# Kernel optimization log

Measured on AMD Instinct MI355X. Metric: run time of the kernel, lower is better.

The kernel has to match this reference:

```python
import jax, jax.numpy as jnp
import numpy as np

SPANS = [15, 9, 5]   # processed largest-first, matching sorted(span_groups, reverse=True)
DEPTH = 2
TOL = 1.5


def _rmsnorm(x, eps=1e-5):
    return x * jax.lax.rsqrt(jnp.mean(x * x, axis=-1, keepdims=True) + eps)


def _block(m, g, Wi, Wz, Wdt, bdt, alog, Wo, Wyg):
    """Dual-input gated selective-scan block (stand-in for create_multihead_block
    block_type='dual_input'): match stream runs a diagonal SSM scan over window
    tokens, gated by the geometry stream; both streams are residually updated."""
    u = _rmsnorm(m) @ Wi                              # [P,L,C]
    z = jax.nn.silu(_rmsnorm(g) @ Wz)                 # [P,L,C] geom gate
    delta = jax.nn.softplus(u @ Wdt + bdt)            # [P,L,C]
    decay = jnp.exp(delta * (-jnp.exp(alog)))         # [P,L,C]
    x_in = delta * u

    def step(h, inp):
        d, xi = inp
        h = d * h + xi
        return h, h

    _, hs = jax.lax.scan(step, jnp.zeros_like(x_in[:, 0]),
                         (jnp.swapaxes(decay, 0, 1), jnp.swapaxes(x_in, 0, 1)))
    y = jnp.swapaxes(hs, 0, 1) * z                    # [P,L,C]
    return m + y @ Wo, g + jax.nn.silu(y @ Wyg)


def _sample(feat_flat, ys, xs, H, W):
    """Bilinear sampling, align_corners=True, padding_mode='zeros'.
    feat_flat: [C, H*W]; ys, xs: [L] float coords. Returns [L, C]."""
    y0 = jnp.floor(ys); x0 = jnp.floor(xs)
    wy = ys - y0; wx = xs - x0

    def tap(yi, xi):
        valid = ((yi >= 0) & (yi <= H - 1) & (xi >= 0) & (xi <= W - 1)).astype(feat_flat.dtype)
        idx = (jnp.clip(yi, 0, H - 1).astype(jnp.int32) * W
               + jnp.clip(xi, 0, W - 1).astype(jnp.int32))
        return feat_flat[:, idx] * valid              # [C,L]

    v = (tap(y0, x0) * (1 - wy) * (1 - wx) + tap(y0, x0 + 1) * (1 - wy) * wx
         + tap(y0 + 1, x0) * wy * (1 - wx) + tap(y0 + 1, x0 + 1) * wy * wx)
    return v.T


def _process_side(feat_m, feat_g, flow, sx, sy, params):
    B, C, H, W = feat_m.shape
    G = feat_g.shape[1]
    Wi, Wz, Wdt, bdt, alog, Wo, Wyg = params
    dt = feat_m.dtype
    bb, yy, xx = [a.ravel() for a in jnp.meshgrid(jnp.arange(B), jnp.arange(H), jnp.arange(W), indexing='ij')]
    # flow-shifted sub-pixel window centers, clamped (flow[...,0]=dx, flow[...,1]=dy)
    cy = jnp.clip(yy.astype(dt) + flow[bb, yy, xx, 1], 0, H - 1)
    cx = jnp.clip(xx.astype(dt) + flow[bb, yy, xx, 0], 0, W - 1)
    avg = ((sx + sy) * 0.5).ravel()
    assigned = jnp.zeros(avg.shape, dtype=bool)
    fm = feat_m.reshape(B, C, H * W)
    fg = feat_g.reshape(B, G, H * W)
    out_m = jnp.zeros((B * H * W, C), dt)
    out_g = jnp.zeros((B * H * W, G), dt)
    wsum = jnp.zeros((B * H * W,), dt)
    for si, s in enumerate(SPANS):
        # span-group mask; positions claimed by a larger span are excluded
        mask = (jnp.abs(avg - s) < TOL) & (~assigned)
        assigned = assigned | mask
        h = s // 2
        dy, dx = [a.ravel() for a in jnp.meshgrid(jnp.arange(-h, h + 1), jnp.arange(-h, h + 1), indexing='ij')]
        dist = jnp.sqrt((dy * dy + dx * dx).astype(dt))
        pw = jnp.exp(-dist / (s / 2.0))
        pw = pw / pw.sum()                             # normalized distance weights [L]
        ys = cy[:, None] + dy[None, :].astype(dt)      # [P,L]
        xs = cx[:, None] + dx[None, :].astype(dt)
        wm = jax.vmap(lambda b, y, x: _sample(fm[b], y, x, H, W))(bb, ys, xs)  # [P,L,C]
        wg = jax.vmap(lambda b, y, x: _sample(fg[b], y, x, H, W))(bb, ys, xs)  # [P,L,G]
        for d in range(DEPTH):
            wm, wg = _block(wm, wg, Wi[si, d], Wz[si, d], Wdt[si, d], bdt[si, d], alog[si, d], Wo[si, d], Wyg[si, d])
        # scatter-accumulate around the integer center position
        ty = yy[:, None] + dy[None, :]
        tx = xx[:, None] + dx[None, :]
        valid = ((ty >= 0) & (ty < H) & (tx >= 0) & (tx < W)).astype(dt)
        w = pw[None, :] * mask[:, None].astype(dt) * valid           # [P,L]
        idx = bb[:, None] * (H * W) + jnp.clip(ty, 0, H - 1) * W + jnp.clip(tx, 0, W - 1)
        out_m = out_m.at[idx.ravel()].add((wm * w[..., None]).reshape(-1, C))
        out_g = out_g.at[idx.ravel()].add((wg * w[..., None]).reshape(-1, G))
        wsum = wsum.at[idx.ravel()].add(w.ravel())
    ws = jnp.maximum(wsum, 1e-6)[:, None]
    om = (out_m / ws).reshape(B, H, W, C).transpose(0, 3, 1, 2)
    og = (out_g / ws).reshape(B, H, W, G).transpose(0, 3, 1, 2)
    return om, og


def setup_inputs() -> dict:
    key = jax.random.key(0)
    ks = jax.random.split(key, 18)
    B, C, G, H, W = 1, 128, 64, 28, 28
    f32 = jnp.float32
    d = {}
    d['feat_match_0'] = jax.random.normal(ks[0], (B, C, H, W), f32)
    d['feat_match_1'] = jax.random.normal(ks[1], (B, C, H, W), f32)
    d['feat_geom_0'] = jax.random.normal(ks[2], (B, G, H, W), f32)
    d['feat_geom_1'] = jax.random.normal(ks[3], (B, G, H, W), f32)
    d['flow_map_0'] = 1.5 * jax.random.normal(ks[4], (B, H, W, 4), f32)
    d['flow_map_1'] = 1.5 * jax.random.normal(ks[5], (B, H, W, 4), f32)
    # spans in [3, 17) so each span group {5, 9, 15} is populated
    d['adaptive_spans_x_0'] = 3.0 + 14.0 * jax.random.uniform(ks[6], (B, H, W), f32)
    d['adaptive_spans_y_0'] = 3.0 + 14.0 * jax.random.uniform(ks[7], (B, H, W), f32)
    d['adaptive_spans_x_1'] = 3.0 + 14.0 * jax.random.uniform(ks[8], (B, H, W), f32)
    d['adaptive_spans_y_1'] = 3.0 + 14.0 * jax.random.uniform(ks[9], (B, H, W), f32)
    # per-span (order [15,9,5]) x per-depth block parameters
    d['W_in'] = jax.random.normal(ks[10], (3, DEPTH, C, C), f32) / np.sqrt(C).astype(np.float32)
    d['W_z'] = jax.random.normal(ks[11], (3, DEPTH, G, C), f32) / np.sqrt(G).astype(np.float32)
    d['W_dt'] = jax.random.normal(ks[12], (3, DEPTH, C, C), f32) / np.sqrt(C).astype(np.float32)
    d['b_dt'] = 0.1 * jax.random.normal(ks[13], (3, DEPTH, C), f32)
    d['a_log'] = 0.1 * jax.random.normal(ks[14], (3, DEPTH, C), f32)
    d['W_out'] = jax.random.normal(ks[15], (3, DEPTH, C, C), f32) / np.sqrt(C).astype(np.float32)
    d['W_yg'] = jax.random.normal(ks[16], (3, DEPTH, C, G), f32) / np.sqrt(C).astype(np.float32)
    return d


def reference(feat_match_0, feat_match_1, feat_geom_0, feat_geom_1,
              flow_map_0, flow_map_1,
              adaptive_spans_x_0, adaptive_spans_y_0,
              adaptive_spans_x_1, adaptive_spans_y_1,
              W_in, W_z, W_dt, b_dt, a_log, W_out, W_yg):
    params = (W_in, W_z, W_dt, b_dt, a_log, W_out, W_yg)
    m0, g0 = _process_side(feat_match_0, feat_geom_0, flow_map_0[..., :2],
                           adaptive_spans_x_0, adaptive_spans_y_0, params)
    m1, g1 = _process_side(feat_match_1, feat_geom_1, flow_map_1[..., :2],
                           adaptive_spans_x_1, adaptive_spans_y_1, params)
    return m0, m1, g0, g1
```

## Files before the change

kernel.cpp:

```cpp
#include <hip/hip_runtime.h>
#include <math.h>

typedef short s16x8 __attribute__((ext_vector_type(8)));
typedef unsigned short u16x8v __attribute__((ext_vector_type(8)));
typedef float f32x4 __attribute__((ext_vector_type(4)));
typedef _Float16 h2 __attribute__((ext_vector_type(2)));

#define HH 28
#define WW 28
#define PP 784
#define CC 128
#define GG 64
#define MT 48
#define NH 3
#define AST 136
#define GSTB 72

#define OFF_FMT0 0
#define OFF_FMT1 100352
#define OFF_FGT0 200704
#define OFF_FGT1 250880
#define OFF_ACCM0 301056
#define OFF_ACCM1 401408
#define OFF_ACCG0 501760
#define OFF_ACCG1 551936
#define OFF_ACCW0 602112
#define OFF_ACCW1 602896
#define ACC_FLOATS 302624
#define OFF_CNT   603680
#define OFF_CNT2  603704
#define OFF_JOB   603728
#define OFF_WB    605296

#define WIB 0
#define WZB 98304
#define WDB 147456
#define WOB 245760
#define WYB 344064

struct KArgs {
  const float* fm[2]; const float* fg[2];
  const float* flow[2]; const float* sx[2]; const float* sy[2];
  const float* Wi; const float* Wz; const float* Wdt; const float* bdt;
  const float* alog; const float* Wo; const float* Wyg;
  float* fmT[2]; float* fgT[2];
  float* accm[2]; float* accg[2]; float* accw[2];
  int* cnt; int* cnt2; int* job;
  unsigned short* wb;
  float* out;
};

__device__ __forceinline__ int span_group(float avg, int& s) {
  if (fabsf(avg - 15.f) < 1.5f) { s = 15; return 0; }
  if (fabsf(avg - 9.f)  < 1.5f) { s = 9;  return 1; }
  if (fabsf(avg - 5.f)  < 1.5f) { s = 5;  return 2; }
  s = 0; return 3;
}

__device__ __forceinline__ float fast_silu(float x) {
  return x * __builtin_amdgcn_rcpf(1.f + __expf(-x));
}

__device__ __forceinline__ unsigned short f2bf(float f) {
  unsigned u = __float_as_uint(f);
  unsigned r = (u + 0x7fffu + ((u >> 16) & 1u)) >> 16;
  return (unsigned short)r;
}
__device__ __forceinline__ float b2f(unsigned short u) {
  return __uint_as_float(((unsigned)u) << 16);
}

__device__ __forceinline__ void atomic_pk2(_Float16* base, float x, float y) {
  h2 v; v[0] = (_Float16)x; v[1] = (_Float16)y;
#if __has_builtin(__builtin_amdgcn_global_atomic_fadd_v2f16)
  __builtin_amdgcn_global_atomic_fadd_v2f16((h2*)base, v);
#else
  unsigned* a = (unsigned*)base;
  unsigned old = *a, assumed;
  do {
    assumed = old;
    h2 cur = *(h2*)&assumed;
    h2 nw; nw[0] = cur[0] + v[0]; nw[1] = cur[1] + v[1];
    old = atomicCAS(a, assumed, *(unsigned*)&nw);
  } while (old != assumed);
#endif
}

#define MFMA(A_, B_, C_) __builtin_amdgcn_mfma_f32_16x16x32_bf16((A_), (B_), (C_), 0, 0, 0)

__global__ void k_zero(float* p, int n) {
  int j = blockIdx.x * 256 + threadIdx.x;
  if (j < n) p[j] = 0.f;
}

__global__ void k_prep(KArgs a) {
  int j = blockIdx.x * 256 + threadIdx.x;
  int side = j / 150528; int r = j - side * 150528;
  int p = r / 192; int ch = r - p * 192;
  if (ch < CC) a.fmT[side][p * CC + ch] = a.fm[side][ch * PP + p];
  else         a.fgT[side][p * GG + (ch - CC)] = a.fg[side][(ch - CC) * PP + p];
}

__global__ void k_prepw(KArgs a) {
  int j = blockIdx.x * 256 + threadIdx.x;
  unsigned short* wb = a.wb;
  if (j < 98304) {
    int set = j >> 14, r = j & 16383; int o = r >> 7, c = r & 127;
    wb[WIB + j] = f2bf(a.Wi[set * 16384 + c * 128 + o]);
  } else if (j < 147456) {
    int r = j - 98304; int set = r >> 13, rr = r & 8191; int o = rr >> 6, c = rr & 63;
    wb[WZB + r] = f2bf(a.Wz[set * 8192 + c * 128 + o]);
  } else if (j < 245760) {
  } else if (j < 344064) {
    int r = j - 245760; int set = r >> 14, rr = r & 16383; int o = rr >> 7, c = rr & 127;
    wb[WOB + r] = f2bf(a.Wo[set * 16384 + c * 128 + o]);
  } else {
    int r = j - 344064; int set = r >> 13, rr = r & 8191; int o = rr >> 7, c = rr & 127;
    wb[WYB + r] = f2bf(a.Wyg[set * 8192 + c * 64 + o]);
  }
}

__global__ void k_prepwid(KArgs a) {
  __shared__ float wi_row[128];
  const int set = blockIdx.x, i = blockIdx.y, o = threadIdx.x;
  wi_row[o] = a.Wi[set * 16384 + i * 128 + o];
  __syncthreads();
  float acc = 0.f;
#pragma unroll 4
  for (int m = 0; m < 128; ++m) acc = fmaf(wi_row[m], a.Wdt[set * 16384 + m * 128 + o], acc);
  a.wb[WDB + set * 16384 + o * 128 + i] = f2bf(acc);
}

__global__ void k_count(KArgs a) {
  int j = blockIdx.x * 256 + threadIdx.x;
  if (j >= 2 * PP) return;
  a.job[j] = -1;
  int side = j / PP, p = j - side * PP;
  float avg = 0.5f * (a.sx[side][p] + a.sy[side][p]);
  int s; int g = span_group(avg, s);
  if (g < 3) {
    int py = p / WW, px = p - py * WW;
    int region = (py / 14) * 4 + px / 7;
    atomicAdd(&a.cnt[region * 3 + g], 1);
  }
}

__global__ void k_assign(KArgs a) {
  int j = blockIdx.x * 256 + threadIdx.x;
  if (j >= 2 * PP) return;
  int side = j / PP, p = j - side * PP;
  float avg = 0.5f * (a.sx[side][p] + a.sy[side][p]);
  int s; int g = span_group(avg, s);
  if (g < 3) {
    int py = p / WW, px = p - py * WW;
    int region = (py / 14) * 4 + px / 7;
    int base = 0;
    for (int gg = 0; gg < g; ++gg) base += a.cnt[region * 3 + gg];
    int rank = base + atomicAdd(&a.cnt2[region * 3 + g], 1);
    a.job[region + 8 * rank] = (side << 10) | p;
  }
}

__global__ void k_fin(KArgs a) {
  int j = blockIdx.x * 256 + threadIdx.x;
  int side = j / 150528; int r = j - side * 150528;
  int p = r / 192; int ch = r - p * 192;
  float inv = 1.f / fmaxf(a.accw[side][p], 1e-6f);
  if (ch < CC) {
    const _Float16* amh = (const _Float16*)a.accm[side];
    a.out[side * 100352 + ch * PP + p] = (float)amh[p * CC + ch] * inv;
  } else {
    const _Float16* agh = (const _Float16*)a.accg[side];
    a.out[200704 + side * 50176 + (ch - CC) * PP + p] = (float)agh[p * GG + (ch - CC)] * inv;
  }
}

__launch_bounds__(256, 3)
__global__ void k_main(KArgs a) {
  __shared__ __align__(16) unsigned short mres[MT * AST];
  __shared__ __align__(16) unsigned short gres[MT * GSTB];
  __shared__ __align__(16) unsigned short bufA[MT * AST];
  __shared__ __align__(16) unsigned short bufB[MT * GSTB];
  __shared__ float hs[2 * CC];
  __shared__ float na_s[2 * CC];
  __shared__ float bb_s[2 * CC];
  __shared__ float pw_l[228];
  __shared__ int   tap_i[MT * 4];
  __shared__ float tap_w[MT * 4];
  __shared__ int   sc_i[MT];
  __shared__ float sc_w[MT];
  __shared__ float red[4];

  const int tid = threadIdx.x;
  const int job = a.job[blockIdx.x];
  if (job < 0) return;
  const int side = job >> 10, p = job & 1023;
  const float avg = 0.5f * (a.sx[side][p] + a.sy[side][p]);
  int s; const int si = span_group(avg, s);
  const int hspan = s >> 1, L = s * s;
  const int py = p / WW, px = p - py * WW;
  const float fdx = a.flow[side][p * 4 + 0], fdy = a.flow[side][p * 4 + 1];
  const float cy = fminf(fmaxf((float)py + fdy, 0.f), (float)(HH - 1));
  const float cx = fminf(fmaxf((float)px + fdx, 0.f), (float)(WW - 1));
  const float* fmT = a.fmT[side]; const float* fgT = a.fgT[side];
  _Float16* accm_h = (_Float16*)a.accm[side];
  _Float16* accg_h = (_Float16*)a.accg[side];
  float* accw = a.accw[side];

  const unsigned short* wb = a.wb;
  const int wv = tid >> 6, l = tid & 63, lm = l & 15, g = l >> 4;
  const int o0 = 32 * wv + lm, o1 = o0 + 16, og = 16 * wv + lm;
  const int ttk = tid >> 3, c8 = tid & 7;

  { const int d2 = tid >> 7, c2 = tid & 127;
    na_s[tid] = -__expf(a.alog[(si * 2 + d2) * CC + c2]);
    bb_s[tid] = a.bdt[(si * 2 + d2) * CC + c2];
    hs[tid] = 0.f; }
  if (tid < L) {
    const int dyi = tid / s - hspan, dxi = tid % s - hspan;
    pw_l[tid] = __expf(-sqrtf((float)(dyi * dyi + dxi * dxi)) / (0.5f * (float)s));
  }
  __syncthreads();
  { float v = (tid < L) ? pw_l[tid] : 0.f;
#pragma unroll
    for (int off = 32; off > 0; off >>= 1) v += __shfl_xor(v, off);
    if ((tid & 63) == 0) red[tid >> 6] = v; }
  __syncthreads();
  { const float pinv = 1.f / (red[0] + red[1] + red[2] + red[3]);
    if (tid < L) pw_l[tid] *= pinv; }
  __syncthreads();

  const int nt = (L + MT - 1) / MT;

  for (int t = 0; t < nt; ++t) {
    const int t0 = t * MT;
    const int tlen = min(MT, L - t0);
    if (tid < MT) {
      const int t2 = t0 + tid;
      if (t2 < L) {
        const int tq = t2 / s;
        const int dyi = tq - hspan, dxi = (t2 - tq * s) - hspan;
        const float ys = cy + (float)dyi, xs = cx + (float)dxi;
        const float y0f = floorf(ys), x0f = floorf(xs);
        const float wy = ys - y0f, wx = xs - x0f;
        const int y0 = (int)y0f, x0 = (int)x0f;
#pragma unroll
        for (int k = 0; k < 4; ++k) {
          const int yi = y0 + (k >> 1), xi = x0 + (k & 1);
          const bool v = (yi >= 0) && (yi < HH) && (xi >= 0) && (xi < WW);
          const int yc = min(max(yi, 0), HH - 1), xc = min(max(xi, 0), WW - 1);
          tap_i[tid * 4 + k] = yc * WW + xc;
          const float wgt = ((k >> 1) ? wy : 1.f - wy) * ((k & 1) ? wx : 1.f - wx);
          tap_w[tid * 4 + k] = v ? wgt : 0.f;
        }
        const int ty = py + dyi, tx = px + dxi;
        const bool sv = (ty >= 0) && (ty < HH) && (tx >= 0) && (tx < WW);
        const int sid2 = sv ? ty * WW + tx : 0;
        const float sw = sv ? pw_l[t2] : 0.f;
        sc_i[tid] = sid2; sc_w[tid] = sw;
        if (sw != 0.f) atomicAdd(&accw[sid2], sw);
      } else {
#pragma unroll
        for (int k = 0; k < 4; ++k) { tap_i[tid * 4 + k] = 0; tap_w[tid * 4 + k] = 0.f; }
        sc_i[tid] = 0; sc_w[tid] = 0.f;
      }
    }
    __syncthreads();
    for (int tk = ttk; tk < MT; tk += 32) {
      const int* ti = &tap_i[tk * 4]; const float* tw = &tap_w[tk * 4];
      f32x4 am0 = {0.f,0.f,0.f,0.f}, am1 = am0, am2 = am0, am3 = am0;
      f32x4 ag0 = am0, ag1 = am0;
#pragma unroll
      for (int k2 = 0; k2 < 4; ++k2) {
        const float w = tw[k2];
        const float* pm = &fmT[ti[k2] * CC + c8 * 16];
        am0 += w * *(const f32x4*)&pm[0];
        am1 += w * *(const f32x4*)&pm[4];
        am2 += w * *(const f32x4*)&pm[8];
        am3 += w * *(const f32x4*)&pm[12];
        const float* pg = &fgT[ti[k2] * GG + c8 * 8];
        ag0 += w * *(const f32x4*)&pg[0];
        ag1 += w * *(const f32x4*)&pg[4];
      }
      u16x8v w0, w1, wg;
#pragma unroll
      for (int j = 0; j < 4; ++j) {
        w0[j] = f2bf(am0[j]); w0[4 + j] = f2bf(am1[j]);
        w1[j] = f2bf(am2[j]); w1[4 + j] = f2bf(am3[j]);
        wg[j] = f2bf(ag0[j]); wg[4 + j] = f2bf(ag1[j]);
      }
      *(u16x8v*)&mres[tk * AST + c8 * 16] = w0;
      *(u16x8v*)&mres[tk * AST + c8 * 16 + 8] = w1;
      *(u16x8v*)&gres[tk * GSTB + c8 * 8] = wg;
    }

    for (int d = 0; d < 2; ++d) {
      const unsigned short* Wib  = wb + WIB + (si * 2 + d) * 16384;
      const unsigned short* Widb = wb + WDB + (si * 2 + d) * 16384;
      const unsigned short* Wzb  = wb + WZB + (si * 2 + d) * 8192;
      const unsigned short* Wob  = wb + WOB + (si * 2 + d) * 16384;
      const unsigned short* Wyb  = wb + WYB + (si * 2 + d) * 8192;
      if (d == 1) __syncthreads();
      for (int tk = ttk; tk < MT; tk += 32) {
        u16x8v m0 = *(const u16x8v*)&mres[tk * AST + c8 * 16];
        u16x8v m1 = *(const u16x8v*)&mres[tk * AST + c8 * 16 + 8];
        u16x8v gv = *(const u16x8v*)&gres[tk * GSTB + c8 * 8];
        float mv[16], gvf[8];
#pragma unroll
        for (int k = 0; k < 8; ++k) { mv[k] = b2f(m0[k]); mv[8 + k] = b2f(m1[k]); gvf[k] = b2f(gv[k]); }
        float ssm = 0.f, ssg = 0.f;
#pragma unroll
        for (int k = 0; k < 16; ++k) ssm = fmaf(mv[k], mv[k], ssm);
#pragma unroll
        for (int k = 0; k < 8; ++k) ssg = fmaf(gvf[k], gvf[k], ssg);
#pragma unroll
        for (int off = 4; off > 0; off >>= 1) { ssm += __shfl_xor(ssm, off); ssg += __shfl_xor(ssg, off); }
        const float sm = rsqrtf(ssm * (1.f / CC) + 1e-5f);
        const float sgs = rsqrtf(ssg * (1.f / GG) + 1e-5f);
        u16x8v xa, xb, gx;
#pragma unroll
        for (int k = 0; k < 8; ++k) { xa[k] = f2bf(mv[k] * sm); xb[k] = f2bf(mv[8 + k] * sm); gx[k] = f2bf(gvf[k] * sgs); }
        *(u16x8v*)&bufA[tk * AST + c8 * 16] = xa;
        *(u16x8v*)&bufA[tk * AST + c8 * 16 + 8] = xb;
        *(u16x8v*)&bufB[tk * GSTB + c8 * 8] = gx;
      }
      __syncthreads();
      f32x4 u[NH][2], dt[NH][2], z[NH][2];
#pragma unroll
      for (int h = 0; h < NH; ++h)
#pragma unroll
        for (int j2 = 0; j2 < 2; ++j2) { u[h][j2] = (f32x4){0.f,0.f,0.f,0.f}; dt[h][j2] = (f32x4){0.f,0.f,0.f,0.f}; z[h][j2] = (f32x4){0.f,0.f,0.f,0.f}; }
#pragma unroll
      for (int ss = 0; ss < 4; ++ss) {
        const int c0 = 32 * ss + g * 8;
        const s16x8 bW0 = *(const s16x8*)&Wib[o0 * 128 + c0];
        const s16x8 bW1 = *(const s16x8*)&Wib[o1 * 128 + c0];
        const s16x8 bD0 = *(const s16x8*)&Widb[o0 * 128 + c0];
        const s16x8 bD1 = *(const s16x8*)&Widb[o1 * 128 + c0];
#pragma unroll
        for (int h = 0; h < NH; ++h) {
          s16x8 av = *(const s16x8*)&bufA[(h * 16 + lm) * AST + c0];
          u[h][0]  = MFMA(av, bW0, u[h][0]);
          u[h][1]  = MFMA(av, bW1, u[h][1]);
          dt[h][0] = MFMA(av, bD0, dt[h][0]);
          dt[h][1] = MFMA(av, bD1, dt[h][1]);
        }
      }
#pragma unroll
      for (int ss = 0; ss < 2; ++ss) {
        const int c0 = 32 * ss + g * 8;
        const s16x8 bZ0 = *(const s16x8*)&Wzb[o0 * 64 + c0];
        const s16x8 bZ1 = *(const s16x8*)&Wzb[o1 * 64 + c0];
#pragma unroll
        for (int h = 0; h < NH; ++h) {
          s16x8 gv2 = *(const s16x8*)&bufB[(h * 16 + lm) * GSTB + c0];
          z[h][0] = MFMA(gv2, bZ0, z[h][0]);
          z[h][1] = MFMA(gv2, bZ1, z[h][1]);
        }
      }
#pragma unroll
      for (int h = 0; h < NH; ++h)
#pragma unroll
        for (int j2 = 0; j2 < 2; ++j2)
#pragma unroll
          for (int r = 0; r < 4; ++r) z[h][j2][r] = fast_silu(z[h][j2][r]);

#pragma unroll
      for (int j2 = 0; j2 < 2; ++j2) {
        const int oc = j2 ? o1 : o0;
        const float bb = bb_s[d * CC + oc], na = na_s[d * CC + oc];
        float hcar = hs[d * CC + oc];
#pragma unroll
        for (int h = 0; h < NH; ++h) {
          float Pl[4], Dl[4]; float P = 0.f, D = 1.f;
#pragma unroll
          for (int r = 0; r < 4; ++r) {
            const float x = dt[h][j2][r] + bb;
            float dlt = fmaxf(x, 0.f) + __logf(1.f + __expf(-fabsf(x)));
            float dec = __expf(dlt * na), xin = dlt * u[h][j2][r];
            if (h * 16 + 4 * g + r >= tlen) { dec = 1.f; xin = 0.f; }
            P = dec * P + xin; D *= dec; Pl[r] = P; Dl[r] = D;
          }
          float Pi = P, Di = D;
          { float pa = __shfl_up(Pi, 16), da = __shfl_up(Di, 16);
            if (g >= 1) { Pi = Di * pa + Pi; Di *= da; }
            pa = __shfl_up(Pi, 32); da = __shfl_up(Di, 32);
            if (g >= 2) { Pi = Di * pa + Pi; Di *= da; } }
          float Pe = __shfl_up(Pi, 16), De = __shfl_up(Di, 16);
          if (g == 0) { Pe = 0.f; De = 1.f; }
          const float cr = De * hcar + Pe;
          const float Pf = __shfl(Pi, 48 + lm), Df = __shfl(Di, 48 + lm);
#pragma unroll
          for (int r = 0; r < 4; ++r) z[h][j2][r] = (Dl[r] * cr + Pl[r]) * z[h][j2][r];
          hcar = Df * hcar + Pf;
        }
        if (g == 0) hs[d * CC + oc] = hcar;
      }
      __syncthreads();
#pragma unroll
      for (int h = 0; h < NH; ++h)
#pragma unroll
        for (int r = 0; r < 4; ++r) {
          const int rw = h * 16 + 4 * g + r;
          bufA[rw * AST + o0] = f2bf(z[h][0][r]);
          bufA[rw * AST + o1] = f2bf(z[h][1][r]);
        }
      __syncthreads();
      f32x4 dm[NH][2], dgv[NH];
#pragma unroll
      for (int h = 0; h < NH; ++h) { dm[h][0] = (f32x4){0.f,0.f,0.f,0.f}; dm[h][1] = (f32x4){0.f,0.f,0.f,0.f}; dgv[h] = (f32x4){0.f,0.f,0.f,0.f}; }
#pragma unroll
      for (int ss = 0; ss < 4; ++ss) {
        const int c0 = 32 * ss + g * 8;
        const s16x8 bO0 = *(const s16x8*)&Wob[o0 * 128 + c0];
        const s16x8 bO1 = *(const s16x8*)&Wob[o1 * 128 + c0];
        const s16x8 bY  = *(const s16x8*)&Wyb[og * 128 + c0];
#pragma unroll
        for (int h = 0; h < NH; ++h) {
          s16x8 av = *(const s16x8*)&bufA[(h * 16 + lm) * AST + c0];
          dm[h][0] = MFMA(av, bO0, dm[h][0]);
          dm[h][1] = MFMA(av, bO1, dm[h][1]);
          dgv[h]   = MFMA(av, bY, dgv[h]);
        }
      }
      if (d == 0) {
#pragma unroll
        for (int h = 0; h < NH; ++h)
#pragma unroll
          for (int r = 0; r < 4; ++r) {
            const int rw = h * 16 + 4 * g + r;
            mres[rw * AST + o0] = f2bf(b2f(mres[rw * AST + o0]) + dm[h][0][r]);
            mres[rw * AST + o1] = f2bf(b2f(mres[rw * AST + o1]) + dm[h][1][r]);
            gres[rw * GSTB + og] = f2bf(b2f(gres[rw * GSTB + og]) + fast_silu(dgv[h][r]));
          }
      } else {
        const bool evn = (lm & 1) == 0;
#pragma unroll
        for (int h = 0; h < NH; ++h)
#pragma unroll
          for (int r = 0; r < 4; ++r) {
            const int rw = h * 16 + 4 * g + r;
            const float w = sc_w[rw];
            const int tgt = sc_i[rw];
            const float vm0 = (b2f(mres[rw * AST + o0]) + dm[h][0][r]) * w;
            const float vm1 = (b2f(mres[rw * AST + o1]) + dm[h][1][r]) * w;
            const float vg  = (b2f(gres[rw * GSTB + og]) + fast_silu(dgv[h][r])) * w;
            const float pm0 = __shfl_xor(vm0, 1);
            const float pm1 = __shfl_xor(vm1, 1);
            const float pg  = __shfl_xor(vg, 1);
            if (w != 0.f) {
              if (evn) {
                atomic_pk2(accm_h + tgt * CC + o0, vm0, pm0);
                atomic_pk2(accg_h + tgt * GG + og, vg, pg);
              } else {
                atomic_pk2(accm_h + tgt * CC + o1 - 1, pm1, vm1);
              }
            }
          }
      }
    }
    __syncthreads();
  }
}

extern "C" void kernel_launch(void* const* d_in, const int* in_sizes, int n_in,
                              void* d_out, int out_size, void* d_ws, size_t ws_size,
                              hipStream_t stream) {
  (void)in_sizes; (void)n_in; (void)out_size; (void)ws_size;
  float* ws = (float*)d_ws;
  KArgs a;
  a.fm[0]  = (const float*)d_in[0]; a.fm[1]  = (const float*)d_in[1];
  a.fg[0]  = (const float*)d_in[2]; a.fg[1]  = (const float*)d_in[3];
  a.flow[0] = (const float*)d_in[4]; a.flow[1] = (const float*)d_in[5];
  a.sx[0] = (const float*)d_in[6]; a.sy[0] = (const float*)d_in[7];
  a.sx[1] = (const float*)d_in[8]; a.sy[1] = (const float*)d_in[9];
  a.Wi  = (const float*)d_in[10]; a.Wz   = (const float*)d_in[11];
  a.Wdt = (const float*)d_in[12]; a.bdt  = (const float*)d_in[13];
  a.alog = (const float*)d_in[14]; a.Wo  = (const float*)d_in[15];
  a.Wyg = (const float*)d_in[16];
  a.fmT[0] = ws + OFF_FMT0; a.fmT[1] = ws + OFF_FMT1;
  a.fgT[0] = ws + OFF_FGT0; a.fgT[1] = ws + OFF_FGT1;
  a.accm[0] = ws + OFF_ACCM0; a.accm[1] = ws + OFF_ACCM1;
  a.accg[0] = ws + OFF_ACCG0; a.accg[1] = ws + OFF_ACCG1;
  a.accw[0] = ws + OFF_ACCW0; a.accw[1] = ws + OFF_ACCW1;
  a.cnt  = (int*)(ws + OFF_CNT);
  a.cnt2 = (int*)(ws + OFF_CNT2);
  a.job  = (int*)(ws + OFF_JOB);
  a.wb   = (unsigned short*)(ws + OFF_WB);
  a.out = (float*)d_out;

  k_zero<<<1183, 256, 0, stream>>>(ws + OFF_ACCM0, ACC_FLOATS);
  k_zero<<<1, 256, 0, stream>>>(ws + OFF_CNT, 48);
  k_prep<<<1176, 256, 0, stream>>>(a);
  k_prepw<<<1536, 256, 0, stream>>>(a);
  k_prepwid<<<dim3(6, 128), 128, 0, stream>>>(a);
  k_count<<<7, 256, 0, stream>>>(a);
  k_assign<<<7, 256, 0, stream>>>(a);
  k_main<<<1568, 256, 0, stream>>>(a);
  k_fin<<<1176, 256, 0, stream>>>(a);
}
```

Baseline: 201.2 us.

## Double k_main block to 512 threads with one output column tile per wave

Raises k_main from 256 to 512 threads so each of 8 waves owns a single 16-column output slice instead of two, halving per-thread MFMA accumulators and weight loads. The W_yg GEMM and geometry updates run only on the first four waves, and the gather and norm loops become single iterations per thread. The aim is more waves in flight and lower register pressure per thread for latency hiding. The cost is idle waves during the geometry-stream work and more threads contending at barriers.

```diff
diff --git a/kernel.cpp b/kernel.cpp
--- a/kernel.cpp
+++ b/kernel.cpp
@@ -175,7 +175,7 @@
   }
 }
 
-__launch_bounds__(256, 3)
+__launch_bounds__(512, 6)
 __global__ void k_main(KArgs a) {
   __shared__ __align__(16) unsigned short mres[MT * AST];
   __shared__ __align__(16) unsigned short gres[MT * GSTB];
@@ -189,7 +189,7 @@
   __shared__ float tap_w[MT * 4];
   __shared__ int   sc_i[MT];
   __shared__ float sc_w[MT];
-  __shared__ float red[4];
+  __shared__ float red[8];
 
   const int tid = threadIdx.x;
   const int job = a.job[blockIdx.x];
@@ -209,13 +209,15 @@
 
   const unsigned short* wb = a.wb;
   const int wv = tid >> 6, l = tid & 63, lm = l & 15, g = l >> 4;
-  const int o0 = 32 * wv + lm, o1 = o0 + 16, og = 16 * wv + lm;
+  const int o = 16 * wv + lm;
   const int ttk = tid >> 3, c8 = tid & 7;
 
-  { const int d2 = tid >> 7, c2 = tid & 127;
+  if (tid < 256) {
+    const int d2 = tid >> 7, c2 = tid & 127;
     na_s[tid] = -__expf(a.alog[(si * 2 + d2) * CC + c2]);
     bb_s[tid] = a.bdt[(si * 2 + d2) * CC + c2];
-    hs[tid] = 0.f; }
+    hs[tid] = 0.f;
+  }
   if (tid < L) {
     const int dyi = tid / s - hspan, dxi = tid % s - hspan;
     pw_l[tid] = __expf(-sqrtf((float)(dyi * dyi + dxi * dxi)) / (0.5f * (float)s));
@@ -226,8 +228,10 @@
     for (int off = 32; off > 0; off >>= 1) v += __shfl_xor(v, off);
     if ((tid & 63) == 0) red[tid >> 6] = v; }
   __syncthreads();
-  { const float pinv = 1.f / (red[0] + red[1] + red[2] + red[3]);
-    if (tid < L) pw_l[tid] *= pinv; }
+  { float tot = 0.f;
+#pragma unroll
+    for (int k = 0; k < 8; ++k) tot += red[k];
+    if (tid < L) pw_l[tid] *= (1.f / tot); }
   __syncthreads();
 
   const int nt = (L + MT - 1) / MT;
@@ -266,8 +270,8 @@
       }
     }
     __syncthreads();
-    for (int tk = ttk; tk < MT; tk += 32) {
-      const int* ti = &tap_i[tk * 4]; const float* tw = &tap_w[tk * 4];
+    if (ttk < MT) {
+      const int* ti = &tap_i[ttk * 4]; const float* tw = &tap_w[ttk * 4];
       f32x4 am0 = {0.f,0.f,0.f,0.f}, am1 = am0, am2 = am0, am3 = am0;
       f32x4 ag0 = am0, ag1 = am0;
 #pragma unroll
@@ -289,9 +293,9 @@
         w1[j] = f2bf(am2[j]); w1[4 + j] = f2bf(am3[j]);
         wg[j] = f2bf(ag0[j]); wg[4 + j] = f2bf(ag1[j]);
       }
-      *(u16x8v*)&mres[tk * AST + c8 * 16] = w0;
-      *(u16x8v*)&mres[tk * AST + c8 * 16 + 8] = w1;
-      *(u16x8v*)&gres[tk * GSTB + c8 * 8] = wg;
+      *(u16x8v*)&mres[ttk * AST + c8 * 16] = w0;
+      *(u16x8v*)&mres[ttk * AST + c8 * 16 + 8] = w1;
+      *(u16x8v*)&gres[ttk * GSTB + c8 * 8] = wg;
     }
 
     for (int d = 0; d < 2; ++d) {
@@ -301,10 +305,10 @@
       const unsigned short* Wob  = wb + WOB + (si * 2 + d) * 16384;
       const unsigned short* Wyb  = wb + WYB + (si * 2 + d) * 8192;
       if (d == 1) __syncthreads();
-      for (int tk = ttk; tk < MT; tk += 32) {
-        u16x8v m0 = *(const u16x8v*)&mres[tk * AST + c8 * 16];
-        u16x8v m1 = *(const u16x8v*)&mres[tk * AST + c8 * 16 + 8];
-        u16x8v gv = *(const u16x8v*)&gres[tk * GSTB + c8 * 8];
+      if (ttk < MT) {
+        u16x8v m0 = *(const u16x8v*)&mres[ttk * AST + c8 * 16];
+        u16x8v m1 = *(const u16x8v*)&mres[ttk * AST + c8 * 16 + 8];
+        u16x8v gv = *(const u16x8v*)&gres[ttk * GSTB + c8 * 8];
         float mv[16], gvf[8];
 #pragma unroll
         for (int k = 0; k < 8; ++k) { mv[k] = b2f(m0[k]); mv[8 + k] = b2f(m1[k]); gvf[k] = b2f(gv[k]); }
@@ -320,64 +324,51 @@
         u16x8v xa, xb, gx;
 #pragma unroll
         for (int k = 0; k < 8; ++k) { xa[k] = f2bf(mv[k] * sm); xb[k] = f2bf(mv[8 + k] * sm); gx[k] = f2bf(gvf[k] * sgs); }
-        *(u16x8v*)&bufA[tk * AST + c8 * 16] = xa;
-        *(u16x8v*)&bufA[tk * AST + c8 * 16 + 8] = xb;
-        *(u16x8v*)&bufB[tk * GSTB + c8 * 8] = gx;
+        *(u16x8v*)&bufA[ttk * AST + c8 * 16] = xa;
+        *(u16x8v*)&bufA[ttk * AST + c8 * 16 + 8] = xb;
+        *(u16x8v*)&bufB[ttk * GSTB + c8 * 8] = gx;
       }
       __syncthreads();
-      f32x4 u[NH][2], dt[NH][2], z[NH][2];
-#pragma unroll
-      for (int h = 0; h < NH; ++h)
-#pragma unroll
-        for (int j2 = 0; j2 < 2; ++j2) { u[h][j2] = (f32x4){0.f,0.f,0.f,0.f}; dt[h][j2] = (f32x4){0.f,0.f,0.f,0.f}; z[h][j2] = (f32x4){0.f,0.f,0.f,0.f}; }
+      f32x4 u[NH], dt[NH], z[NH];
+#pragma unroll
+      for (int h = 0; h < NH; ++h) { u[h] = (f32x4){0.f,0.f,0.f,0.f}; dt[h] = (f32x4){0.f,0.f,0.f,0.f}; z[h] = (f32x4){0.f,0.f,0.f,0.f}; }
 #pragma unroll
       for (int ss = 0; ss < 4; ++ss) {
         const int c0 = 32 * ss + g * 8;
-        const s16x8 bW0 = *(const s16x8*)&Wib[o0 * 128 + c0];
-        const s16x8 bW1 = *(const s16x8*)&Wib[o1 * 128 + c0];
-        const s16x8 bD0 = *(const s16x8*)&Widb[o0 * 128 + c0];
-        const s16x8 bD1 = *(const s16x8*)&Widb[o1 * 128 + c0];
+        const s16x8 bW = *(const s16x8*)&Wib[o * 128 + c0];
+        const s16x8 bD = *(const s16x8*)&Widb[o * 128 + c0];
 #pragma unroll
         for (int h = 0; h < NH; ++h) {
           s16x8 av = *(const s16x8*)&bufA[(h * 16 + lm) * AST + c0];
-          u[h][0]  = MFMA(av, bW0, u[h][0]);
-          u[h][1]  = MFMA(av, bW1, u[h][1]);
-          dt[h][0] = MFMA(av, bD0, dt[h][0]);
-          dt[h][1] = MFMA(av, bD1, dt[h][1]);
+          u[h]  = MFMA(av, bW, u[h]);
+          dt[h] = MFMA(av, bD, dt[h]);
         }
       }
 #pragma unroll
       for (int ss = 0; ss < 2; ++ss) {
         const int c0 = 32 * ss + g * 8;
-        const s16x8 bZ0 = *(const s16x8*)&Wzb[o0 * 64 + c0];
-        const s16x8 bZ1 = *(const s16x8*)&Wzb[o1 * 64 + c0];
+        const s16x8 bZ = *(const s16x8*)&Wzb[o * 64 + c0];
 #pragma unroll
         for (int h = 0; h < NH; ++h) {
           s16x8 gv2 = *(const s16x8*)&bufB[(h * 16 + lm) * GSTB + c0];
-          z[h][0] = MFMA(gv2, bZ0, z[h][0]);
-          z[h][1] = MFMA(gv2, bZ1, z[h][1]);
+          z[h] = MFMA(gv2, bZ, z[h]);
         }
       }
 #pragma unroll
       for (int h = 0; h < NH; ++h)
 #pragma unroll
-        for (int j2 = 0; j2 < 2; ++j2)
-#pragma unroll
-          for (int r = 0; r < 4; ++r) z[h][j2][r] = fast_silu(z[h][j2][r]);
-
-#pragma unroll
-      for (int j2 = 0; j2 < 2; ++j2) {
-        const int oc = j2 ? o1 : o0;
-        const float bb = bb_s[d * CC + oc], na = na_s[d * CC + oc];
-        float hcar = hs[d * CC + oc];
+        for (int r = 0; r < 4; ++r) z[h][r] = fast_silu(z[h][r]);
+
+      { const float bb = bb_s[d * CC + o], na = na_s[d * CC + o];
+        float hcar = hs[d * CC + o];
 #pragma unroll
         for (int h = 0; h < NH; ++h) {
           float Pl[4], Dl[4]; float P = 0.f, D = 1.f;
 #pragma unroll
           for (int r = 0; r < 4; ++r) {
-            const float x = dt[h][j2][r] + bb;
+            const float x = dt[h][r] + bb;
             float dlt = fmaxf(x, 0.f) + __logf(1.f + __expf(-fabsf(x)));
-            float dec = __expf(dlt * na), xin = dlt * u[h][j2][r];
+            float dec = __expf(dlt * na), xin = dlt * u[h][r];
             if (h * 16 + 4 * g + r >= tlen) { dec = 1.f; xin = 0.f; }
             P = dec * P + xin; D *= dec; Pl[r] = P; Dl[r] = D;
           }
@@ -391,36 +382,41 @@
           const float cr = De * hcar + Pe;
           const float Pf = __shfl(Pi, 48 + lm), Df = __shfl(Di, 48 + lm);
 #pragma unroll
-          for (int r = 0; r < 4; ++r) z[h][j2][r] = (Dl[r] * cr + Pl[r]) * z[h][j2][r];
+          for (int r = 0; r < 4; ++r) z[h][r] = (Dl[r] * cr + Pl[r]) * z[h][r];
           hcar = Df * hcar + Pf;
         }
-        if (g == 0) hs[d * CC + oc] = hcar;
+        if (g == 0) hs[d * CC + o] = hcar;
       }
       __syncthreads();
 #pragma unroll
       for (int h = 0; h < NH; ++h)
 #pragma unroll
-        for (int r = 0; r < 4; ++r) {
-          const int rw = h * 16 + 4 * g + r;
-          bufA[rw * AST + o0] = f2bf(z[h][0][r]);
-          bufA[rw * AST + o1] = f2bf(z[h][1][r]);
-        }
+        for (int r = 0; r < 4; ++r)
+          bufA[(h * 16 + 4 * g + r) * AST + o] = f2bf(z[h][r]);
       __syncthreads();
-      f32x4 dm[NH][2], dgv[NH];
-#pragma unroll
-      for (int h = 0; h < NH; ++h) { dm[h][0] = (f32x4){0.f,0.f,0.f,0.f}; dm[h][1] = (f32x4){0.f,0.f,0.f,0.f}; dgv[h] = (f32x4){0.f,0.f,0.f,0.f}; }
+      f32x4 dm[NH], dgv[NH];
+#pragma unroll
+      for (int h = 0; h < NH; ++h) { dm[h] = (f32x4){0.f,0.f,0.f,0.f}; dgv[h] = (f32x4){0.f,0.f,0.f,0.f}; }
 #pragma unroll
       for (int ss = 0; ss < 4; ++ss) {
         const int c0 = 32 * ss + g * 8;
-        const s16x8 bO0 = *(const s16x8*)&Wob[o0 * 128 + c0];
-        const s16x8 bO1 = *(const s16x8*)&Wob[o1 * 128 + c0];
-        const s16x8 bY  = *(const s16x8*)&Wyb[og * 128 + c0];
+        const s16x8 bO = *(const s16x8*)&Wob[o * 128 + c0];
 #pragma unroll
         for (int h = 0; h < NH; ++h) {
           s16x8 av = *(const s16x8*)&bufA[(h * 16 + lm) * AST + c0];
-          dm[h][0] = MFMA(av, bO0, dm[h][0]);
-          dm[h][1] = MFMA(av, bO1, dm[h][1]);
-          dgv[h]   = MFMA(av, bY, dgv[h]);
+          dm[h] = MFMA(av, bO, dm[h]);
+        }
+      }
+      if (wv < 4) {
+#pragma unroll
+        for (int ss = 0; ss < 4; ++ss) {
+          const int c0 = 32 * ss + g * 8;
+          const s16x8 bY = *(const s16x8*)&Wyb[o * 128 + c0];
+#pragma unroll
+          for (int h = 0; h < NH; ++h) {
+            s16x8 av = *(const s16x8*)&bufA[(h * 16 + lm) * AST + c0];
+            dgv[h] = MFMA(av, bY, dgv[h]);
+          }
         }
       }
       if (d == 0) {
@@ -429,9 +425,8 @@
 #pragma unroll
           for (int r = 0; r < 4; ++r) {
             const int rw = h * 16 + 4 * g + r;
-            mres[rw * AST + o0] = f2bf(b2f(mres[rw * AST + o0]) + dm[h][0][r]);
-            mres[rw * AST + o1] = f2bf(b2f(mres[rw * AST + o1]) + dm[h][1][r]);
-            gres[rw * GSTB + og] = f2bf(b2f(gres[rw * GSTB + og]) + fast_silu(dgv[h][r]));
+            mres[rw * AST + o] = f2bf(b2f(mres[rw * AST + o]) + dm[h][r]);
+            if (wv < 4) gres[rw * GSTB + o] = f2bf(b2f(gres[rw * GSTB + o]) + fast_silu(dgv[h][r]));
           }
       } else {
         const bool evn = (lm & 1) == 0;
@@ -442,19 +437,14 @@
             const int rw = h * 16 + 4 * g + r;
             const float w = sc_w[rw];
             const int tgt = sc_i[rw];
-            const float vm0 = (b2f(mres[rw * AST + o0]) + dm[h][0][r]) * w;
-            const float vm1 = (b2f(mres[rw * AST + o1]) + dm[h][1][r]) * w;
-            const float vg  = (b2f(gres[rw * GSTB + og]) + fast_silu(dgv[h][r])) * w;
-            const float pm0 = __shfl_xor(vm0, 1);
-            const float pm1 = __shfl_xor(vm1, 1);
-            const float pg  = __shfl_xor(vg, 1);
-            if (w != 0.f) {
-              if (evn) {
-                atomic_pk2(accm_h + tgt * CC + o0, vm0, pm0);
-                atomic_pk2(accg_h + tgt * GG + og, vg, pg);
-              } else {
-                atomic_pk2(accm_h + tgt * CC + o1 - 1, pm1, vm1);
-              }
+            const float vm = (b2f(mres[rw * AST + o]) + dm[h][r]) * w;
+            const float pm = __shfl_xor(vm, 1);
+            float vg = 0.f;
+            if (wv < 4) vg = (b2f(gres[rw * GSTB + o]) + fast_silu(dgv[h][r])) * w;
+            const float pg = __shfl_xor(vg, 1);
+            if (w != 0.f && evn) {
+              atomic_pk2(accm_h + tgt * CC + o, vm, pm);
+              if (wv < 4) atomic_pk2(accg_h + tgt * GG + o, vg, pg);
             }
           }
       }
@@ -496,6 +486,6 @@
   k_prepwid<<<dim3(6, 128), 128, 0, stream>>>(a);
   k_count<<<7, 256, 0, stream>>>(a);
   k_assign<<<7, 256, 0, stream>>>(a);
-  k_main<<<1568, 256, 0, stream>>>(a);
+  k_main<<<1568, 512, 0, stream>>>(a);
   k_fin<<<1176, 256, 0, stream>>>(a);
 }
```

Result: slower. 296.3 us (+47.3%).
